# Optimization experiments

Hardware: AMD Instinct MI355X
Metric: run time of the kernel (lower is better)

Reference implementation:

```python
import jax, jax.numpy as jnp
import numpy as np

D_Z = 1024
D_MODEL = 4096
EPS = 1e-5  # torch LayerNorm default
CLAMP = 3.0


def setup_inputs() -> dict:
    key = jax.random.key(0)
    k_z, k_w, k_b = jax.random.split(key, 3)
    z = jax.random.normal(k_z, (8, 2048, D_Z), dtype=jnp.float32)
    # LayerNorm params (gamma=1, beta=0 init in torch; keep learnable form)
    ln_gamma = jnp.ones((D_Z,), dtype=jnp.float32)
    ln_beta = jnp.zeros((D_Z,), dtype=jnp.float32)
    # Linear: torch default init U(-1/sqrt(d_z), 1/sqrt(d_z))
    bound = 1.0 / np.sqrt(D_Z)
    W = jax.random.uniform(k_w, (D_Z, D_MODEL), minval=-bound, maxval=bound, dtype=jnp.float32)
    b = jax.random.uniform(k_b, (D_MODEL,), minval=-bound, maxval=bound, dtype=jnp.float32)
    scale = jnp.ones((1,), dtype=jnp.float32)
    return {"z": z, "ln_gamma": ln_gamma, "ln_beta": ln_beta, "W": W, "b": b, "scale": scale}


def reference(z, ln_gamma, ln_beta, W, b, scale):
    # LayerNorm over last dim
    mu = jnp.mean(z, axis=-1, keepdims=True)
    var = jnp.mean(jnp.square(z - mu), axis=-1, keepdims=True)
    zn = (z - mu) * jax.lax.rsqrt(var + EPS) * ln_gamma + ln_beta
    # Linear -> scalar scale -> tanh clamp
    x = (jnp.einsum('bsd,dm->bsm', zn, W) + b) * scale
    return jnp.tanh(x / CLAMP) * CLAMP
```

## Files before the change

kernel.cpp:

```cpp
#include <hip/hip_runtime.h>

#define M_DIM 16384
#define K_DIM 1024
#define N_DIM 4096
#define T_TILES (K_DIM / 32)

typedef __bf16 bf16x8 __attribute__((ext_vector_type(8)));
typedef float f32x16 __attribute__((ext_vector_type(16)));

__device__ __forceinline__ unsigned short f2bf(float f) {
    union { float f; unsigned int i; } v; v.f = f;
    unsigned int r = v.i + 0x7fffu + ((v.i >> 16) & 1u);
    return (unsigned short)(r >> 16);
}
__device__ __forceinline__ unsigned int pack2(float lo, float hi) {
    return ((unsigned int)f2bf(lo)) | (((unsigned int)f2bf(hi)) << 16);
}

__global__ __launch_bounds__(256) void ln_kernel(
        const float* __restrict__ z,
        const float* __restrict__ gamma,
        const float* __restrict__ beta,
        unsigned short* __restrict__ zn) {
    const int wave = threadIdx.x >> 6;
    const int lane = threadIdx.x & 63;
    const size_t row = (size_t)blockIdx.x * 4 + wave;
    const float* zr = z + row * K_DIM;

    float4 x[4];
#pragma unroll
    for (int v = 0; v < 4; v++) x[v] = *(const float4*)(zr + v * 256 + lane * 4);

    float s = 0.f, ss = 0.f;
#pragma unroll
    for (int v = 0; v < 4; v++) {
        s  += x[v].x + x[v].y + x[v].z + x[v].w;
        ss += x[v].x * x[v].x + x[v].y * x[v].y + x[v].z * x[v].z + x[v].w * x[v].w;
    }
#pragma unroll
    for (int o = 32; o; o >>= 1) { s += __shfl_xor(s, o, 64); ss += __shfl_xor(ss, o, 64); }
    const float mean = s * (1.f / K_DIM);
    const float var = ss * (1.f / K_DIM) - mean * mean;
    const float rstd = rsqrtf(var + 1e-5f);

#pragma unroll
    for (int v = 0; v < 4; v++) {
        float4 g = *(const float4*)(gamma + v * 256 + lane * 4);
        float4 b = *(const float4*)(beta + v * 256 + lane * 4);
        float o0 = (x[v].x - mean) * rstd * g.x + b.x;
        float o1 = (x[v].y - mean) * rstd * g.y + b.y;
        float o2 = (x[v].z - mean) * rstd * g.z + b.z;
        float o3 = (x[v].w - mean) * rstd * g.w + b.w;
        uint2 q; q.x = pack2(o0, o1); q.y = pack2(o2, o3);
        *(uint2*)(zn + row * K_DIM + v * 256 + lane * 4) = q;
    }
}

__global__ __launch_bounds__(256) void tr_kernel(
        const float* __restrict__ W, unsigned short* __restrict__ Wt) {
    __shared__ float t[32][33];
    const int tx = threadIdx.x, ty = threadIdx.y;
    const int n0 = blockIdx.x * 32, k0 = blockIdx.y * 32;
#pragma unroll
    for (int j = 0; j < 32; j += 8)
        t[ty + j][tx] = W[(size_t)(k0 + ty + j) * N_DIM + n0 + tx];
    __syncthreads();
#pragma unroll
    for (int j = 0; j < 32; j += 8)
        Wt[(size_t)(n0 + ty + j) * K_DIM + k0 + tx] = f2bf(t[tx][ty + j]);
}

__device__ __forceinline__ void async_copy16(const unsigned short* g, unsigned short* l) {
    __builtin_amdgcn_global_load_lds(
        (const __attribute__((address_space(1))) unsigned int*)g,
        (__attribute__((address_space(3))) unsigned int*)l,
        16, 0, 0);
}

__global__ __launch_bounds__(512, 2) void gemm_kernel(
        const unsigned short* __restrict__ A,
        const unsigned short* __restrict__ B,
        const float* __restrict__ bias,
        const float* __restrict__ scale,
        float* __restrict__ out) {
    __shared__ __align__(16) unsigned short As[4][256 * 32];
    __shared__ __align__(16) unsigned short Bs[4][256 * 32];

    const int tid = threadIdx.x;
    const int wave = tid >> 6, lane = tid & 63;
    const int wm = wave >> 2, wn = wave & 3;
    const int l31 = lane & 31, lhi = lane >> 5;

    const int bid = blockIdx.y * gridDim.x + blockIdx.x;
    const int id2 = (bid & 7) * 128 + (bid >> 3);
    const int bm = id2 >> 4, bn = id2 & 15;

    const int r0 = tid >> 2;
    const int c0 = ((tid & 3) ^ ((tid >> 3) & 3)) << 3;
    const unsigned short* agA = A + (size_t)(bm * 256 + r0) * K_DIM + c0;
    const unsigned short* agB = B + (size_t)(bn * 256 + r0) * K_DIM + c0;
    const int ldsu = wave * 512;

#define STAGE_A(t_, s_) do { \
        const unsigned short* g_ = agA + (t_) * 32; \
        async_copy16(g_,                 &As[s_][ldsu]); \
        async_copy16(g_ + 128 * K_DIM,   &As[s_][4096 + ldsu]); } while (0)
#define STAGE_B(t_, s_) do { \
        const unsigned short* g_ = agB + (t_) * 32; \
        async_copy16(g_,                 &Bs[s_][ldsu]); \
        async_copy16(g_ + 128 * K_DIM,   &Bs[s_][4096 + ldsu]); } while (0)

    f32x16 acc[4][2] = {};
    const int swz = (l31 >> 1) & 3;

    STAGE_A(0, 0); STAGE_B(0, 0);
    STAGE_A(1, 1); STAGE_B(1, 1);
    STAGE_A(2, 2); STAGE_B(2, 2);

#pragma unroll 4
    for (int t = 0; t < T_TILES; ++t) {
        const int s = t & 3;
        const int ts = t + 3, ss = ts & 3;

        if (t <= T_TILES - 3)      asm volatile("s_waitcnt vmcnt(8)" ::: "memory");
        else if (t == T_TILES - 2) asm volatile("s_waitcnt vmcnt(4)" ::: "memory");
        else                       asm volatile("s_waitcnt vmcnt(0)" ::: "memory");
        __builtin_amdgcn_s_barrier();
        asm volatile("" ::: "memory");

        const unsigned short* as_ = As[s];
        const unsigned short* bs_ = Bs[s];
        bf16x8 a[2][2], b[2][2];

#pragma unroll
        for (int i = 0; i < 2; ++i)
#pragma unroll
            for (int ks = 0; ks < 2; ++ks)
                a[i][ks] = *(const bf16x8*)&as_[(wm * 128 + i * 32 + l31) * 32 + (((2 * ks + lhi) ^ swz) << 3)];
#pragma unroll
        for (int j = 0; j < 2; ++j)
#pragma unroll
            for (int ks = 0; ks < 2; ++ks)
                b[j][ks] = *(const bf16x8*)&bs_[(wn * 64 + j * 32 + l31) * 32 + (((2 * ks + lhi) ^ swz) << 3)];
        if (ts < T_TILES) STAGE_A(ts, ss);
        __builtin_amdgcn_s_setprio(1);
#pragma unroll
        for (int i = 0; i < 2; ++i)
#pragma unroll
            for (int j = 0; j < 2; ++j)
#pragma unroll
                for (int ks = 0; ks < 2; ++ks)
                    acc[i][j] = __builtin_amdgcn_mfma_f32_32x32x16_bf16(a[i][ks], b[j][ks], acc[i][j], 0, 0, 0);
        __builtin_amdgcn_s_setprio(0);
        asm volatile("" ::: "memory");
        __builtin_amdgcn_s_barrier();
        asm volatile("" ::: "memory");

#pragma unroll
        for (int i = 0; i < 2; ++i)
#pragma unroll
            for (int ks = 0; ks < 2; ++ks)
                a[i][ks] = *(const bf16x8*)&as_[(wm * 128 + 64 + i * 32 + l31) * 32 + (((2 * ks + lhi) ^ swz) << 3)];
        if (ts < T_TILES) STAGE_B(ts, ss);
        __builtin_amdgcn_s_setprio(1);
#pragma unroll
        for (int i = 0; i < 2; ++i)
#pragma unroll
            for (int j = 0; j < 2; ++j)
#pragma unroll
                for (int ks = 0; ks < 2; ++ks)
                    acc[2 + i][j] = __builtin_amdgcn_mfma_f32_32x32x16_bf16(a[i][ks], b[j][ks], acc[2 + i][j], 0, 0, 0);
        __builtin_amdgcn_s_setprio(0);
        asm volatile("" ::: "memory");
    }
#undef STAGE_A
#undef STAGE_B

    const float mfac = scale[0] * 0.96179669392236f;
#pragma unroll
    for (int j = 0; j < 2; ++j) {
        const int gcol = bn * 256 + wn * 64 + j * 32 + l31;
        const float bv = bias[gcol];
#pragma unroll
        for (int i = 0; i < 4; ++i) {
            const int rbase = bm * 256 + wm * 128 + i * 32 + 4 * lhi;
#pragma unroll
            for (int r = 0; r < 16; ++r) {
                const int grow = rbase + (r & 3) + 8 * (r >> 2);
                float tv = (acc[i][j][r] + bv) * mfac;
                float e = __builtin_amdgcn_exp2f(tv);
                out[(size_t)grow * N_DIM + gcol] = 3.f - 6.f * __builtin_amdgcn_rcpf(e + 1.f);
            }
        }
    }
}

extern "C" void kernel_launch(void* const* d_in, const int* in_sizes, int n_in,
                              void* d_out, int out_size, void* d_ws, size_t ws_size,
                              hipStream_t stream) {
    const float* z     = (const float*)d_in[0];
    const float* gamma = (const float*)d_in[1];
    const float* beta  = (const float*)d_in[2];
    const float* W     = (const float*)d_in[3];
    const float* b     = (const float*)d_in[4];
    const float* scale = (const float*)d_in[5];
    float* out = (float*)d_out;

    unsigned short* zn = (unsigned short*)d_ws;
    unsigned short* Wt = zn + (size_t)M_DIM * K_DIM;

    ln_kernel<<<M_DIM / 4, 256, 0, stream>>>(z, gamma, beta, zn);
    tr_kernel<<<dim3(N_DIM / 32, K_DIM / 32), dim3(32, 8), 0, stream>>>(W, Wt);
    gemm_kernel<<<dim3(N_DIM / 256, M_DIM / 256), 512, 0, stream>>>(zn, Wt, b, scale, out);
}
```

Before: 463.8 us.

## Merge LN and transpose kernels; software-pipeline LDS fragment reads in GEMM

The LayerNorm and weight-transpose kernels are merged into one launch, with the block index choosing the role, which saves a launch and lets both run concurrently. In the GEMM main loop, the LDS fragment reads for the next tile and for the second half of the current tile are moved ahead of the barriers, so they overlap with MFMA work. Explicit lgkmcnt waits and sched_barriers fix the ordering, and the MFMA loop order now runs ks outermost. The restructured vmcnt and barrier sequence adds risk of extra stalls or ordering mistakes.

```diff
diff --git a/kernel.cpp b/kernel.cpp
--- a/kernel.cpp
+++ b/kernel.cpp
@@ -17,57 +17,60 @@
     return ((unsigned int)f2bf(lo)) | (((unsigned int)f2bf(hi)) << 16);
 }
 
-__global__ __launch_bounds__(256) void ln_kernel(
+__global__ __launch_bounds__(256) void prep_kernel(
         const float* __restrict__ z,
         const float* __restrict__ gamma,
         const float* __restrict__ beta,
-        unsigned short* __restrict__ zn) {
-    const int wave = threadIdx.x >> 6;
-    const int lane = threadIdx.x & 63;
-    const size_t row = (size_t)blockIdx.x * 4 + wave;
-    const float* zr = z + row * K_DIM;
-
-    float4 x[4];
-#pragma unroll
-    for (int v = 0; v < 4; v++) x[v] = *(const float4*)(zr + v * 256 + lane * 4);
-
-    float s = 0.f, ss = 0.f;
-#pragma unroll
-    for (int v = 0; v < 4; v++) {
-        s  += x[v].x + x[v].y + x[v].z + x[v].w;
-        ss += x[v].x * x[v].x + x[v].y * x[v].y + x[v].z * x[v].z + x[v].w * x[v].w;
+        unsigned short* __restrict__ zn,
+        const float* __restrict__ W,
+        unsigned short* __restrict__ Wt) {
+    __shared__ float t[32][33];
+    const int tid = threadIdx.x;
+    if (blockIdx.x < M_DIM / 4) {
+        const int wave = tid >> 6;
+        const int lane = tid & 63;
+        const size_t row = (size_t)blockIdx.x * 4 + wave;
+        const float* zr = z + row * K_DIM;
+
+        float4 x[4];
+#pragma unroll
+        for (int v = 0; v < 4; v++) x[v] = *(const float4*)(zr + v * 256 + lane * 4);
+
+        float s = 0.f, ss = 0.f;
+#pragma unroll
+        for (int v = 0; v < 4; v++) {
+            s  += x[v].x + x[v].y + x[v].z + x[v].w;
+            ss += x[v].x * x[v].x + x[v].y * x[v].y + x[v].z * x[v].z + x[v].w * x[v].w;
+        }
+#pragma unroll
+        for (int o = 32; o; o >>= 1) { s += __shfl_xor(s, o, 64); ss += __shfl_xor(ss, o, 64); }
+        const float mean = s * (1.f / K_DIM);
+        const float var = ss * (1.f / K_DIM) - mean * mean;
+        const float rstd = rsqrtf(var + 1e-5f);
+
+#pragma unroll
+        for (int v = 0; v < 4; v++) {
+            float4 g = *(const float4*)(gamma + v * 256 + lane * 4);
+            float4 b = *(const float4*)(beta + v * 256 + lane * 4);
+            float o0 = (x[v].x - mean) * rstd * g.x + b.x;
+            float o1 = (x[v].y - mean) * rstd * g.y + b.y;
+            float o2 = (x[v].z - mean) * rstd * g.z + b.z;
+            float o3 = (x[v].w - mean) * rstd * g.w + b.w;
+            uint2 q; q.x = pack2(o0, o1); q.y = pack2(o2, o3);
+            *(uint2*)(zn + row * K_DIM + v * 256 + lane * 4) = q;
+        }
+    } else {
+        const int bid = blockIdx.x - M_DIM / 4;
+        const int tx = tid & 31, ty = tid >> 5;
+        const int n0 = (bid & (N_DIM / 32 - 1)) * 32, k0 = (bid / (N_DIM / 32)) * 32;
+#pragma unroll
+        for (int j = 0; j < 32; j += 8)
+            t[ty + j][tx] = W[(size_t)(k0 + ty + j) * N_DIM + n0 + tx];
+        __syncthreads();
+#pragma unroll
+        for (int j = 0; j < 32; j += 8)
+            Wt[(size_t)(n0 + ty + j) * K_DIM + k0 + tx] = f2bf(t[tx][ty + j]);
     }
-#pragma unroll
-    for (int o = 32; o; o >>= 1) { s += __shfl_xor(s, o, 64); ss += __shfl_xor(ss, o, 64); }
-    const float mean = s * (1.f / K_DIM);
-    const float var = ss * (1.f / K_DIM) - mean * mean;
-    const float rstd = rsqrtf(var + 1e-5f);
-
-#pragma unroll
-    for (int v = 0; v < 4; v++) {
-        float4 g = *(const float4*)(gamma + v * 256 + lane * 4);
-        float4 b = *(const float4*)(beta + v * 256 + lane * 4);
-        float o0 = (x[v].x - mean) * rstd * g.x + b.x;
-        float o1 = (x[v].y - mean) * rstd * g.y + b.y;
-        float o2 = (x[v].z - mean) * rstd * g.z + b.z;
-        float o3 = (x[v].w - mean) * rstd * g.w + b.w;
-        uint2 q; q.x = pack2(o0, o1); q.y = pack2(o2, o3);
-        *(uint2*)(zn + row * K_DIM + v * 256 + lane * 4) = q;
-    }
-}
-
-__global__ __launch_bounds__(256) void tr_kernel(
-        const float* __restrict__ W, unsigned short* __restrict__ Wt) {
-    __shared__ float t[32][33];
-    const int tx = threadIdx.x, ty = threadIdx.y;
-    const int n0 = blockIdx.x * 32, k0 = blockIdx.y * 32;
-#pragma unroll
-    for (int j = 0; j < 32; j += 8)
-        t[ty + j][tx] = W[(size_t)(k0 + ty + j) * N_DIM + n0 + tx];
-    __syncthreads();
-#pragma unroll
-    for (int j = 0; j < 32; j += 8)
-        Wt[(size_t)(n0 + ty + j) * K_DIM + k0 + tx] = f2bf(t[tx][ty + j]);
 }
 
 __device__ __forceinline__ void async_copy16(const unsigned short* g, unsigned short* l) {
@@ -112,69 +115,79 @@
 
     f32x16 acc[4][2] = {};
     const int swz = (l31 >> 1) & 3;
+    bf16x8 a[2][2], b[2][2];
+
+#define READ_A(s_, rb_) do { \
+        const unsigned short* as_ = As[s_]; \
+        _Pragma("unroll") \
+        for (int i_ = 0; i_ < 2; ++i_) \
+        _Pragma("unroll") \
+        for (int ks_ = 0; ks_ < 2; ++ks_) \
+            a[i_][ks_] = *(const bf16x8*)&as_[(wm * 128 + (rb_) + i_ * 32 + l31) * 32 + (((2 * ks_ + lhi) ^ swz) << 3)]; } while (0)
+#define READ_B(s_) do { \
+        const unsigned short* bs_ = Bs[s_]; \
+        _Pragma("unroll") \
+        for (int j_ = 0; j_ < 2; ++j_) \
+        _Pragma("unroll") \
+        for (int ks_ = 0; ks_ < 2; ++ks_) \
+            b[j_][ks_] = *(const bf16x8*)&bs_[(wn * 64 + j_ * 32 + l31) * 32 + (((2 * ks_ + lhi) ^ swz) << 3)]; } while (0)
 
     STAGE_A(0, 0); STAGE_B(0, 0);
     STAGE_A(1, 1); STAGE_B(1, 1);
     STAGE_A(2, 2); STAGE_B(2, 2);
+    asm volatile("s_waitcnt vmcnt(8)" ::: "memory");
+    __builtin_amdgcn_s_barrier();
+    asm volatile("" ::: "memory");
+    READ_A(0, 0); READ_B(0);
 
 #pragma unroll 4
     for (int t = 0; t < T_TILES; ++t) {
-        const int s = t & 3;
-        const int ts = t + 3, ss = ts & 3;
-
-        if (t <= T_TILES - 3)      asm volatile("s_waitcnt vmcnt(8)" ::: "memory");
-        else if (t == T_TILES - 2) asm volatile("s_waitcnt vmcnt(4)" ::: "memory");
-        else                       asm volatile("s_waitcnt vmcnt(0)" ::: "memory");
+        const int s = t & 3, sn = (t + 1) & 3, ss = (t + 3) & 3;
+
+        if (t + 3 < T_TILES) STAGE_A(t + 3, ss);
+        asm volatile("" ::: "memory");
         __builtin_amdgcn_s_barrier();
-        asm volatile("" ::: "memory");
-
-        const unsigned short* as_ = As[s];
-        const unsigned short* bs_ = Bs[s];
-        bf16x8 a[2][2], b[2][2];
-
-#pragma unroll
-        for (int i = 0; i < 2; ++i)
-#pragma unroll
-            for (int ks = 0; ks < 2; ++ks)
-                a[i][ks] = *(const bf16x8*)&as_[(wm * 128 + i * 32 + l31) * 32 + (((2 * ks + lhi) ^ swz) << 3)];
-#pragma unroll
-        for (int j = 0; j < 2; ++j)
-#pragma unroll
-            for (int ks = 0; ks < 2; ++ks)
-                b[j][ks] = *(const bf16x8*)&bs_[(wn * 64 + j * 32 + l31) * 32 + (((2 * ks + lhi) ^ swz) << 3)];
-        if (ts < T_TILES) STAGE_A(ts, ss);
+        asm volatile("s_waitcnt lgkmcnt(0)" ::: "memory");
+        __builtin_amdgcn_sched_barrier(0);
         __builtin_amdgcn_s_setprio(1);
 #pragma unroll
-        for (int i = 0; i < 2; ++i)
-#pragma unroll
-            for (int j = 0; j < 2; ++j)
-#pragma unroll
-                for (int ks = 0; ks < 2; ++ks)
+        for (int ks = 0; ks < 2; ++ks)
+#pragma unroll
+            for (int i = 0; i < 2; ++i)
+#pragma unroll
+                for (int j = 0; j < 2; ++j)
                     acc[i][j] = __builtin_amdgcn_mfma_f32_32x32x16_bf16(a[i][ks], b[j][ks], acc[i][j], 0, 0, 0);
         __builtin_amdgcn_s_setprio(0);
+
+        READ_A(s, 64);
+        if (t + 3 < T_TILES) STAGE_B(t + 3, ss);
         asm volatile("" ::: "memory");
         __builtin_amdgcn_s_barrier();
-        asm volatile("" ::: "memory");
-
-#pragma unroll
-        for (int i = 0; i < 2; ++i)
-#pragma unroll
-            for (int ks = 0; ks < 2; ++ks)
-                a[i][ks] = *(const bf16x8*)&as_[(wm * 128 + 64 + i * 32 + l31) * 32 + (((2 * ks + lhi) ^ swz) << 3)];
-        if (ts < T_TILES) STAGE_B(ts, ss);
+        asm volatile("s_waitcnt lgkmcnt(0)" ::: "memory");
+        __builtin_amdgcn_sched_barrier(0);
         __builtin_amdgcn_s_setprio(1);
 #pragma unroll
-        for (int i = 0; i < 2; ++i)
-#pragma unroll
-            for (int j = 0; j < 2; ++j)
-#pragma unroll
-                for (int ks = 0; ks < 2; ++ks)
+        for (int ks = 0; ks < 2; ++ks)
+#pragma unroll
+            for (int i = 0; i < 2; ++i)
+#pragma unroll
+                for (int j = 0; j < 2; ++j)
                     acc[2 + i][j] = __builtin_amdgcn_mfma_f32_32x32x16_bf16(a[i][ks], b[j][ks], acc[2 + i][j], 0, 0, 0);
         __builtin_amdgcn_s_setprio(0);
-        asm volatile("" ::: "memory");
+
+        if (t < T_TILES - 1) {
+            if (t < T_TILES - 3)       asm volatile("s_waitcnt vmcnt(8)" ::: "memory");
+            else if (t == T_TILES - 3) asm volatile("s_waitcnt vmcnt(4)" ::: "memory");
+            else                       asm volatile("s_waitcnt vmcnt(0)" ::: "memory");
+            __builtin_amdgcn_s_barrier();
+            asm volatile("" ::: "memory");
+            READ_A(sn, 0); READ_B(sn);
+        }
     }
 #undef STAGE_A
 #undef STAGE_B
+#undef READ_A
+#undef READ_B
 
     const float mfac = scale[0] * 0.96179669392236f;
 #pragma unroll
@@ -209,7 +222,6 @@
     unsigned short* zn = (unsigned short*)d_ws;
     unsigned short* Wt = zn + (size_t)M_DIM * K_DIM;
 
-    ln_kernel<<<M_DIM / 4, 256, 0, stream>>>(z, gamma, beta, zn);
-    tr_kernel<<<dim3(N_DIM / 32, K_DIM / 32), dim3(32, 8), 0, stream>>>(W, Wt);
+    prep_kernel<<<M_DIM / 4 + (N_DIM / 32) * (K_DIM / 32), 256, 0, stream>>>(z, gamma, beta, zn, W, Wt);
     gemm_kernel<<<dim3(N_DIM / 256, M_DIM / 256), 512, 0, stream>>>(zn, Wt, b, scale, out);
 }
```

New measurement: 464.1 us. No clear change (+0.1%).
